# Optimization experiments

Measured on AMD Instinct MI355X. Metric: run time of the kernel, lower is better.

## Reference

```python
import jax, jax.numpy as jnp
import numpy as np

B, N, F, K, O = 4, 4096, 32, 6, 128


def setup_inputs() -> dict:
    key = jax.random.key(0)
    k1, k2, k3, k4 = jax.random.split(key, 4)
    x = jax.random.normal(k1, (B, N, F), dtype=jnp.float32)
    # dense per-batch (normalized-Laplacian-like) operator; scaled for stable recurrence
    L = jax.random.normal(k2, (B, N, N), dtype=jnp.float32) / np.float32(np.sqrt(N))
    # per-order projection weights lins[k]: in -> out  (stored [K, F, O])
    W = jax.random.normal(k3, (K, F, O), dtype=jnp.float32) * 0.1
    # per-order scalar 1x1 'theta' weights lins_theta[k]
    theta = jax.random.normal(k4, (K,), dtype=jnp.float32) * 0.1
    return {"x": x, "L": L, "W": W, "theta": theta}


def reference(x, L, W, theta):
    # Chebyshev recurrence: T0 = x, T1 = L@x, T_k = 2 L@T_{k-1} - T_{k-2}
    # Each order: elementwise scalar theta_k (the 1x1 Linear) then Linear(F->O), summed.
    k_orders = W.shape[0]
    x0 = x                                                   # [B,N,F]
    out = theta[0] * jnp.einsum('bnf,fo->bno', x0, W[0])     # [B,N,O]
    if k_orders > 1:
        x1 = jnp.matmul(L, x0)                               # [B,N,F]
        out = out + theta[1] * jnp.einsum('bnf,fo->bno', x1, W[1])
    for k in range(2, k_orders):
        x2 = 2.0 * jnp.matmul(L, x1) - x0
        out = out + theta[k] * jnp.einsum('bnf,fo->bno', x2, W[k])
        x0, x1 = x1, x2
    return out
```

## Files before the change

### kernel.cpp

```cpp
#include <hip/hip_runtime.h>

#define N4 4096
#define FF 32
#define KK 6
#define OO 128
#define BB 4

typedef __attribute__((ext_vector_type(8))) short  short8;
typedef __attribute__((ext_vector_type(4))) float  f32x4;
typedef __attribute__((ext_vector_type(4))) int    i32x4;
typedef __attribute__((ext_vector_type(2))) unsigned int u32x2;

__device__ __forceinline__ float b2f(unsigned short h) {
    union { float f; unsigned u; } v; v.u = ((unsigned)h) << 16; return v.f;
}
__device__ __forceinline__ unsigned short f2b(float f) {
    union { float f; unsigned u; } v; v.f = f;
    unsigned r = (v.u + 0x7FFFu + ((v.u >> 16) & 1u)) >> 16;
    return (unsigned short)r;
}

__device__ __forceinline__ long tb_idx(int b, int ks, int half, int lane) {
    return ((((long)b * 128 + ks) * 2 + half) * 64 + lane) * 8;
}

__global__ __launch_bounds__(256) void make_wc(const float* __restrict__ W,
                                               const float* __restrict__ theta,
                                               unsigned short* __restrict__ Wc) {
    int idx = blockIdx.x * 256 + threadIdx.x;
    int k = idx >> 12;
    Wc[idx] = f2b(theta[k] * W[idx]);
}

__global__ __launch_bounds__(256) void x_to_t(const float* __restrict__ x,
                                              unsigned short* __restrict__ T0) {
    __shared__ __align__(16) unsigned short Ol[32][72];
    int tid = threadIdx.x, bid = blockIdx.x;
    int b = bid >> 6; int nc = bid & 63; long n0 = (long)nc * 64;
    int nl = tid >> 2, fg = (tid & 3) * 8;
    const float* src = x + ((long)b * N4 + n0 + nl) * FF + fg;
    f32x4 v0 = *(const f32x4*)src;
    f32x4 v1 = *(const f32x4*)(src + 4);
#pragma unroll
    for (int e = 0; e < 4; ++e) {
        Ol[fg + e][nl]     = f2b(v0[e]);
        Ol[fg + 4 + e][nl] = f2b(v1[e]);
    }
    __syncthreads();
    int ks_l = tid >> 7, half = (tid >> 6) & 1, lane = tid & 63;
    int quad = lane >> 4, l16 = lane & 15;
    int f = half * 16 + l16, nloc = ks_l * 32 + quad * 8;
    *(i32x4*)(T0 + tb_idx(b, nc * 2 + ks_l, half, lane)) = *(const i32x4*)&Ol[f][nloc];
}

__global__ __launch_bounds__(256) void gemm_pass1(const float* __restrict__ L,
                                                  unsigned short* __restrict__ Lb,
                                                  const unsigned short* __restrict__ Tb0,
                                                  float* __restrict__ P) {
    __shared__ __align__(16) unsigned short Sw[4][2][2][64][8];
    int tid = threadIdx.x, bid = blockIdx.x;
    int b = bid >> 8, ms = bid & 255;
    int w = tid >> 6, lane = tid & 63, l16 = lane & 15;
    int rgrp = lane >> 4;
    const float* Ls = L + ((long)b * N4 + ms * 16 + rgrp) * N4 + (long)w * 1024 + l16 * 4;
    int ks_loc_w = l16 >> 3, quad_w = (l16 >> 1) & 3, e0 = (l16 & 1) * 4;
    const unsigned short* Bbase = Tb0 + tb_idx(b, w * 32, 0, lane);
    unsigned short* LbBase = Lb + (((long)(b * 256 + ms) * 128 + w * 32) * 64 + lane) * 8;

    f32x4 acc0 = {0.f,0.f,0.f,0.f}, acc1 = {0.f,0.f,0.f,0.f};
    f32x4 v[4], vn[4];
#pragma unroll
    for (int j = 0; j < 4; ++j) v[j] = *(const f32x4*)(Ls + (long)j * 4 * N4);

    for (int it = 0; it < 16; ++it) {
        if (it + 1 < 16) {
#pragma unroll
            for (int j = 0; j < 4; ++j)
                vn[j] = *(const f32x4*)(Ls + (long)j * 4 * N4 + (it + 1) * 64);
        }
        short8 b00 = *(const short8*)(Bbase + (long)(it * 2 + 0) * 1024);
        short8 b01 = *(const short8*)(Bbase + (long)(it * 2 + 0) * 1024 + 512);
        short8 b10 = *(const short8*)(Bbase + (long)(it * 2 + 1) * 1024);
        short8 b11 = *(const short8*)(Bbase + (long)(it * 2 + 1) * 1024 + 512);
        unsigned short* Sb = &Sw[w][it & 1][0][0][0];
#pragma unroll
        for (int j = 0; j < 4; ++j) {
            u32x2 pk;
            pk[0] = (unsigned)f2b(v[j][0]) | ((unsigned)f2b(v[j][1]) << 16);
            pk[1] = (unsigned)f2b(v[j][2]) | ((unsigned)f2b(v[j][3]) << 16);
            int lane_o = quad_w * 16 + j * 4 + rgrp;
            *(u32x2*)(Sb + (ks_loc_w * 64 + lane_o) * 8 + e0) = pk;
        }
#pragma unroll
        for (int h = 0; h < 2; ++h) {
            short8 af = *(const short8*)(Sb + (h * 64 + lane) * 8);
            *(short8*)(LbBase + (long)(it * 2 + h) * 512) = af;
            acc0 = __builtin_amdgcn_mfma_f32_16x16x32_bf16(af, h ? b10 : b00, acc0, 0, 0, 0);
            acc1 = __builtin_amdgcn_mfma_f32_16x16x32_bf16(af, h ? b11 : b01, acc1, 0, 0, 0);
        }
#pragma unroll
        for (int j = 0; j < 4; ++j) v[j] = vn[j];
    }
    *(f32x4*)(P + ((((long)(w * 4 + b) * 256 + ms) * 2 + 0) * 64 + lane) * 4) = acc0;
    *(f32x4*)(P + ((((long)(w * 4 + b) * 256 + ms) * 2 + 1) * 64 + lane) * 4) = acc1;
}

__global__ __launch_bounds__(256) void gemm_frag(const unsigned short* __restrict__ Lb,
                                                 const unsigned short* __restrict__ Tb,
                                                 float* __restrict__ P) {
    int tid = threadIdx.x, bid = blockIdx.x;
    int b = bid >> 8, ms = bid & 255;
    int s = tid >> 6, lane = tid & 63;
    const unsigned short* Ap = Lb + (((long)(b * 256 + ms) * 128 + s * 32) * 64 + lane) * 8;
    const unsigned short* Bp = Tb + tb_idx(b, s * 32, 0, lane);

    f32x4 acc0 = {0.f,0.f,0.f,0.f}, acc1 = {0.f,0.f,0.f,0.f};
    short8 Ar[4], B0r[4], B1r[4];
#pragma unroll
    for (int i = 0; i < 4; ++i) {
        Ar[i]  = *(const short8*)(Ap + (long)i * 512);
        B0r[i] = *(const short8*)(Bp + (long)i * 1024);
        B1r[i] = *(const short8*)(Bp + (long)i * 1024 + 512);
    }
#pragma unroll 4
    for (int ks = 0; ks < 32; ++ks) {
        int sl = ks & 3;
        short8 a = Ar[sl], b0 = B0r[sl], b1 = B1r[sl];
        if (ks + 4 < 32) {
            Ar[sl]  = *(const short8*)(Ap + (long)(ks + 4) * 512);
            B0r[sl] = *(const short8*)(Bp + (long)(ks + 4) * 1024);
            B1r[sl] = *(const short8*)(Bp + (long)(ks + 4) * 1024 + 512);
        }
        acc0 = __builtin_amdgcn_mfma_f32_16x16x32_bf16(a, b0, acc0, 0, 0, 0);
        acc1 = __builtin_amdgcn_mfma_f32_16x16x32_bf16(a, b1, acc1, 0, 0, 0);
    }
    *(f32x4*)(P + ((((long)(s * 4 + b) * 256 + ms) * 2 + 0) * 64 + lane) * 4) = acc0;
    *(f32x4*)(P + ((((long)(s * 4 + b) * 256 + ms) * 2 + 1) * 64 + lane) * 4) = acc1;
}

__global__ __launch_bounds__(256) void reduce_frag(const float* __restrict__ P,
                                                   const unsigned short* __restrict__ Tpp,
                                                   unsigned short* __restrict__ Tout,
                                                   float a, float c) {
    __shared__ float Sl[32][66];
    int tid = threadIdx.x, bid = blockIdx.x;
    int b = bid >> 6, nc = bid & 63;
#pragma unroll
    for (int i = 0; i < 2; ++i) {
        int fid = i * 256 + tid;
        int ms_l = fid >> 7, h = (fid >> 6) & 1, lane = fid & 63;
        int quad = lane >> 4, l16 = lane & 15;
        long base = ((((long)b * 256 + nc * 4 + ms_l) * 2 + h) * 64 + lane) * 4;
        f32x4 sum = *(const f32x4*)(P + base);
#pragma unroll
        for (int s = 1; s < 4; ++s) {
            f32x4 v = *(const f32x4*)(P + base + (long)s * 524288);
#pragma unroll
            for (int e = 0; e < 4; ++e) sum[e] += v[e];
        }
        int f = h * 16 + l16, nl = ms_l * 16 + quad * 4;
#pragma unroll
        for (int r = 0; r < 4; ++r) Sl[f][nl + r] = sum[r];
    }
    __syncthreads();
    int ks_l = tid >> 7, half = (tid >> 6) & 1, lane = tid & 63;
    int quad = lane >> 4, l16 = lane & 15;
    int f = half * 16 + l16, nl = ks_l * 32 + quad * 8;
    long oidx = tb_idx(b, nc * 2 + ks_l, half, lane);
    const unsigned short* tp = Tpp ? (Tpp + oidx) : nullptr;
    i32x4 pk;
#pragma unroll
    for (int p = 0; p < 4; ++p) {
        float v0 = a * Sl[f][nl + p * 2];
        float v1 = a * Sl[f][nl + p * 2 + 1];
        if (tp) { v0 += c * b2f(tp[p * 2]); v1 += c * b2f(tp[p * 2 + 1]); }
        pk[p] = (unsigned)f2b(v0) | ((unsigned)f2b(v1) << 16);
    }
    *(i32x4*)(Tout + oidx) = pk;
}

__global__ __launch_bounds__(256) void proj(const unsigned short* __restrict__ T,
                                            const unsigned short* __restrict__ Wc,
                                            float* __restrict__ out) {
    __shared__ __align__(16) unsigned short Tl[192][72];
    __shared__ __align__(16) unsigned short Wl[192][64];
    int tid = threadIdx.x, bid = blockIdx.x;
    int b = bid >> 7; int rem = bid & 127;
    int nc = rem >> 1; long n0 = (long)nc * 64; int oh = rem & 1;
    const long T_SLOT = (long)BB * FF * N4;
#pragma unroll
    for (int it = 0; it < 6; ++it) {
        int row = it * 32 + (tid >> 3);
        int col = (tid & 7) * 8;
        int k = row >> 5, f = row & 31;
        int ks = nc * 2 + (col >> 5), half = f >> 4;
        int lane = ((col & 31) >> 3) * 16 + (f & 15);
        *(i32x4*)&Tl[row][col] = *(const i32x4*)(T + (long)k * T_SLOT + tb_idx(b, ks, half, lane));
        *(i32x4*)&Wl[row][col] = *(const i32x4*)(Wc + (long)row * OO + oh * 64 + col);
    }
    __syncthreads();
    int ol = tid & 63;
    int nb = (tid >> 6) * 16;
    float acc[16];
#pragma unroll
    for (int r = 0; r < 16; ++r) acc[r] = 0.f;
    for (int kf = 0; kf < 192; ++kf) {
        float w = b2f(Wl[kf][ol]);
#pragma unroll
        for (int rv = 0; rv < 2; ++rv) {
            short8 tv = *(const short8*)&Tl[kf][nb + rv * 8];
#pragma unroll
            for (int e = 0; e < 8; ++e)
                acc[rv * 8 + e] += b2f((unsigned short)tv[e]) * w;
        }
    }
    int o = oh * 64 + ol;
#pragma unroll
    for (int r = 0; r < 16; ++r)
        out[((long)b * N4 + n0 + nb + r) * OO + o] = acc[r];
}

extern "C" void kernel_launch(void* const* d_in, const int* in_sizes, int n_in,
                              void* d_out, int out_size, void* d_ws, size_t ws_size,
                              hipStream_t stream) {
    const float* x     = (const float*)d_in[0];
    const float* L     = (const float*)d_in[1];
    const float* W     = (const float*)d_in[2];
    const float* theta = (const float*)d_in[3];
    float* out = (float*)d_out;
    char* ws = (char*)d_ws;

    const size_t LB_BYTES = (size_t)BB * N4 * N4 * 2;
    const size_t T_SLOT   = (size_t)BB * FF * N4;
    const size_t T_BYTES  = (size_t)KK * T_SLOT * 2;
    const size_t P_BYTES  = (size_t)4 * BB * N4 * FF * 4;

    unsigned short* Lb = (unsigned short*)ws;
    unsigned short* T  = (unsigned short*)(ws + LB_BYTES);
    float*          P  = (float*)(ws + LB_BYTES + T_BYTES);
    unsigned short* Wc = (unsigned short*)(ws + LB_BYTES + T_BYTES + P_BYTES);

    make_wc<<<96, 256, 0, stream>>>(W, theta, Wc);
    x_to_t<<<256, 256, 0, stream>>>(x, T);

    gemm_pass1<<<1024, 256, 0, stream>>>(L, Lb, T, P);
    reduce_frag<<<256, 256, 0, stream>>>(P, nullptr, T + 1 * T_SLOT, 1.f, 0.f);

    for (int k = 2; k < KK; ++k) {
        gemm_frag<<<1024, 256, 0, stream>>>(Lb, T + (k - 1) * T_SLOT, P);
        reduce_frag<<<256, 256, 0, stream>>>(P, T + (k - 2) * T_SLOT, T + k * T_SLOT, 2.f, -1.f);
    }

    proj<<<512, 256, 0, stream>>>(T, Wc, out);
}
```

Baseline: 535.0 us.

## Fuse split-K reduction and recurrence update into GEMM kernels via shared memory

The four per-wave split-K partial accumulators are now reduced in shared memory inside gemm_pass1 and gemm_frag. The Chebyshev update (a*sum + c*T_{k-2}) and the bf16 pack are applied in-kernel, writing the T fragment directly. This removes the separate reduce_frag launches and the global float partial buffer round trip. The cost is a block-wide barrier and a serial tail where only 64 of 256 threads do the reduction.

```diff
diff --git a/kernel.cpp b/kernel.cpp
--- a/kernel.cpp
+++ b/kernel.cpp
@@ -53,11 +53,46 @@
     *(i32x4*)(T0 + tb_idx(b, nc * 2 + ks_l, half, lane)) = *(const i32x4*)&Ol[f][nloc];
 }
 
+__device__ __forceinline__ void split_reduce_store(const float (*Pr)[2][64][4],
+                                                   int tid, int b, int ms,
+                                                   const unsigned short* __restrict__ Tpp,
+                                                   unsigned short* __restrict__ Tout,
+                                                   float a, float c) {
+    if (tid >= 64) return;
+    int half = tid >> 5, qi = (tid >> 4) & 1, l16 = tid & 15;
+    f32x4 sA = {0.f, 0.f, 0.f, 0.f}, sB = {0.f, 0.f, 0.f, 0.f};
+#pragma unroll
+    for (int ss = 0; ss < 4; ++ss) {
+        f32x4 va = *(const f32x4*)&Pr[ss][half][qi * 32 + l16][0];
+        f32x4 vb = *(const f32x4*)&Pr[ss][half][qi * 32 + 16 + l16][0];
+#pragma unroll
+        for (int e = 0; e < 4; ++e) { sA[e] += va[e]; sB[e] += vb[e]; }
+    }
+    float vals[8] = {sA[0], sA[1], sA[2], sA[3], sB[0], sB[1], sB[2], sB[3]};
+    int lane_o = ((ms & 1) * 2 + qi) * 16 + l16;
+    long oidx = tb_idx(b, ms >> 1, half, lane_o);
+    i32x4 pk;
+    if (Tpp) {
+        short8 tv = *(const short8*)(Tpp + oidx);
+#pragma unroll
+        for (int p = 0; p < 4; ++p)
+            pk[p] = (unsigned)f2b(a * vals[2 * p]     + c * b2f((unsigned short)tv[2 * p]))
+                  | ((unsigned)f2b(a * vals[2 * p + 1] + c * b2f((unsigned short)tv[2 * p + 1])) << 16);
+    } else {
+#pragma unroll
+        for (int p = 0; p < 4; ++p)
+            pk[p] = (unsigned)f2b(a * vals[2 * p])
+                  | ((unsigned)f2b(a * vals[2 * p + 1]) << 16);
+    }
+    *(i32x4*)(Tout + oidx) = pk;
+}
+
 __global__ __launch_bounds__(256) void gemm_pass1(const float* __restrict__ L,
                                                   unsigned short* __restrict__ Lb,
                                                   const unsigned short* __restrict__ Tb0,
-                                                  float* __restrict__ P) {
+                                                  unsigned short* __restrict__ Tout) {
     __shared__ __align__(16) unsigned short Sw[4][2][2][64][8];
+    __shared__ __align__(16) float Pr[4][2][64][4];
     int tid = threadIdx.x, bid = blockIdx.x;
     int b = bid >> 8, ms = bid & 255;
     int w = tid >> 6, lane = tid & 63, l16 = lane & 15;
@@ -101,13 +136,18 @@
 #pragma unroll
         for (int j = 0; j < 4; ++j) v[j] = vn[j];
     }
-    *(f32x4*)(P + ((((long)(w * 4 + b) * 256 + ms) * 2 + 0) * 64 + lane) * 4) = acc0;
-    *(f32x4*)(P + ((((long)(w * 4 + b) * 256 + ms) * 2 + 1) * 64 + lane) * 4) = acc1;
+    *(f32x4*)&Pr[w][0][lane][0] = acc0;
+    *(f32x4*)&Pr[w][1][lane][0] = acc1;
+    __syncthreads();
+    split_reduce_store(Pr, tid, b, ms, nullptr, Tout, 1.f, 0.f);
 }
 
 __global__ __launch_bounds__(256) void gemm_frag(const unsigned short* __restrict__ Lb,
                                                  const unsigned short* __restrict__ Tb,
-                                                 float* __restrict__ P) {
+                                                 const unsigned short* __restrict__ Tpp,
+                                                 unsigned short* __restrict__ Tout,
+                                                 float a, float c) {
+    __shared__ __align__(16) float Pr[4][2][64][4];
     int tid = threadIdx.x, bid = blockIdx.x;
     int b = bid >> 8, ms = bid & 255;
     int s = tid >> 6, lane = tid & 63;
@@ -125,58 +165,19 @@
 #pragma unroll 4
     for (int ks = 0; ks < 32; ++ks) {
         int sl = ks & 3;
-        short8 a = Ar[sl], b0 = B0r[sl], b1 = B1r[sl];
+        short8 aa = Ar[sl], b0 = B0r[sl], b1 = B1r[sl];
         if (ks + 4 < 32) {
             Ar[sl]  = *(const short8*)(Ap + (long)(ks + 4) * 512);
             B0r[sl] = *(const short8*)(Bp + (long)(ks + 4) * 1024);
             B1r[sl] = *(const short8*)(Bp + (long)(ks + 4) * 1024 + 512);
         }
-        acc0 = __builtin_amdgcn_mfma_f32_16x16x32_bf16(a, b0, acc0, 0, 0, 0);
-        acc1 = __builtin_amdgcn_mfma_f32_16x16x32_bf16(a, b1, acc1, 0, 0, 0);
-    }
-    *(f32x4*)(P + ((((long)(s * 4 + b) * 256 + ms) * 2 + 0) * 64 + lane) * 4) = acc0;
-    *(f32x4*)(P + ((((long)(s * 4 + b) * 256 + ms) * 2 + 1) * 64 + lane) * 4) = acc1;
-}
-
-__global__ __launch_bounds__(256) void reduce_frag(const float* __restrict__ P,
-                                                   const unsigned short* __restrict__ Tpp,
-                                                   unsigned short* __restrict__ Tout,
-                                                   float a, float c) {
-    __shared__ float Sl[32][66];
-    int tid = threadIdx.x, bid = blockIdx.x;
-    int b = bid >> 6, nc = bid & 63;
-#pragma unroll
-    for (int i = 0; i < 2; ++i) {
-        int fid = i * 256 + tid;
-        int ms_l = fid >> 7, h = (fid >> 6) & 1, lane = fid & 63;
-        int quad = lane >> 4, l16 = lane & 15;
-        long base = ((((long)b * 256 + nc * 4 + ms_l) * 2 + h) * 64 + lane) * 4;
-        f32x4 sum = *(const f32x4*)(P + base);
-#pragma unroll
-        for (int s = 1; s < 4; ++s) {
-            f32x4 v = *(const f32x4*)(P + base + (long)s * 524288);
-#pragma unroll
-            for (int e = 0; e < 4; ++e) sum[e] += v[e];
-        }
-        int f = h * 16 + l16, nl = ms_l * 16 + quad * 4;
-#pragma unroll
-        for (int r = 0; r < 4; ++r) Sl[f][nl + r] = sum[r];
-    }
-    __syncthreads();
-    int ks_l = tid >> 7, half = (tid >> 6) & 1, lane = tid & 63;
-    int quad = lane >> 4, l16 = lane & 15;
-    int f = half * 16 + l16, nl = ks_l * 32 + quad * 8;
-    long oidx = tb_idx(b, nc * 2 + ks_l, half, lane);
-    const unsigned short* tp = Tpp ? (Tpp + oidx) : nullptr;
-    i32x4 pk;
-#pragma unroll
-    for (int p = 0; p < 4; ++p) {
-        float v0 = a * Sl[f][nl + p * 2];
-        float v1 = a * Sl[f][nl + p * 2 + 1];
-        if (tp) { v0 += c * b2f(tp[p * 2]); v1 += c * b2f(tp[p * 2 + 1]); }
-        pk[p] = (unsigned)f2b(v0) | ((unsigned)f2b(v1) << 16);
-    }
-    *(i32x4*)(Tout + oidx) = pk;
+        acc0 = __builtin_amdgcn_mfma_f32_16x16x32_bf16(aa, b0, acc0, 0, 0, 0);
+        acc1 = __builtin_amdgcn_mfma_f32_16x16x32_bf16(aa, b1, acc1, 0, 0, 0);
+    }
+    *(f32x4*)&Pr[s][0][lane][0] = acc0;
+    *(f32x4*)&Pr[s][1][lane][0] = acc1;
+    __syncthreads();
+    split_reduce_store(Pr, tid, b, ms, Tpp, Tout, a, c);
 }
 
 __global__ __launch_bounds__(256) void proj(const unsigned short* __restrict__ T,
@@ -233,22 +234,20 @@
     const size_t LB_BYTES = (size_t)BB * N4 * N4 * 2;
     const size_t T_SLOT   = (size_t)BB * FF * N4;
     const size_t T_BYTES  = (size_t)KK * T_SLOT * 2;
-    const size_t P_BYTES  = (size_t)4 * BB * N4 * FF * 4;
 
     unsigned short* Lb = (unsigned short*)ws;
     unsigned short* T  = (unsigned short*)(ws + LB_BYTES);
-    float*          P  = (float*)(ws + LB_BYTES + T_BYTES);
-    unsigned short* Wc = (unsigned short*)(ws + LB_BYTES + T_BYTES + P_BYTES);
+    unsigned short* Wc = (unsigned short*)(ws + LB_BYTES + T_BYTES);
 
     make_wc<<<96, 256, 0, stream>>>(W, theta, Wc);
     x_to_t<<<256, 256, 0, stream>>>(x, T);
 
-    gemm_pass1<<<1024, 256, 0, stream>>>(L, Lb, T, P);
-    reduce_frag<<<256, 256, 0, stream>>>(P, nullptr, T + 1 * T_SLOT, 1.f, 0.f);
+    gemm_pass1<<<1024, 256, 0, stream>>>(L, Lb, T, T + 1 * T_SLOT);
 
     for (int k = 2; k < KK; ++k) {
-        gemm_frag<<<1024, 256, 0, stream>>>(Lb, T + (k - 1) * T_SLOT, P);
-        reduce_frag<<<256, 256, 0, stream>>>(P, T + (k - 2) * T_SLOT, T + k * T_SLOT, 2.f, -1.f);
+        gemm_frag<<<1024, 256, 0, stream>>>(Lb, T + (k - 1) * T_SLOT,
+                                            T + (k - 2) * T_SLOT, T + k * T_SLOT,
+                                            2.f, -1.f);
     }
 
     proj<<<512, 256, 0, stream>>>(T, Wc, out);
```

Result: faster. 512.4 us (-4.2%).
